# Kernel optimization log

Hardware: AMD Instinct MI355X
Metric: run time of the kernel (lower is better)

## Reference

```python
import jax, jax.numpy as jnp
import numpy as np

N = 100000      # number of nodes
E = 1600000     # number of (directed) edges, avg degree 16
DIN = 128       # in_features
DOUT = 32       # out_features
SLOPE = 0.2     # leaky relu negative slope


def setup_inputs() -> dict:
    key = jax.random.key(0)
    k1, k2, k3, k4, k5, k6 = jax.random.split(key, 6)
    x = jax.random.normal(k1, (N, DIN), dtype=jnp.float32)
    edge_index = jax.random.randint(k2, (2, E), 0, N, dtype=jnp.int32)
    # W1 (shared with W2 and used as the feature-update matrix W, 'source' mode)
    W1_w = jax.random.normal(k3, (DOUT, DIN), dtype=jnp.float32) / np.float32(np.sqrt(DIN))
    W1_b = jax.random.normal(k4, (DOUT,), dtype=jnp.float32) * 0.01
    a1_w = jax.random.normal(k5, (DOUT,), dtype=jnp.float32) / np.float32(np.sqrt(DOUT))
    a2_w = jax.random.normal(k6, (DOUT,), dtype=jnp.float32) / np.float32(np.sqrt(DOUT))
    return {"x": x, "edge_index": edge_index, "W1_w": W1_w, "W1_b": W1_b,
            "a1_w": a1_w, "a2_w": a2_w}


def reference(x, edge_index, W1_w, W1_b, a1_w, a2_w):
    n = x.shape[0]
    # append self-loops, as in _sparse_attention
    loops = jnp.arange(n, dtype=edge_index.dtype)
    src = jnp.concatenate([edge_index[0], loops])   # rows  (softmax segments)
    dst = jnp.concatenate([edge_index[1], loops])   # cols
    # h = W1(x) (linear, with bias); W2 = W1 (weight sharing), W = W2 ('source')
    h = x @ W1_w.T + W1_b                           # [N, DOUT]
    z = jax.nn.leaky_relu(h, SLOPE)                 # x1 == x2 under weight sharing
    s1 = z @ a1_w                                   # [N] per-node src score
    s2 = z @ a2_w                                   # [N] per-node dst score
    logits = s1[src] + s2[dst]                      # [E+N] per-edge attention logit
    # row-wise (dim=1) sparse softmax == segment softmax over src
    m = jax.ops.segment_max(logits, src, num_segments=n)
    ex = jnp.exp(logits - m[src])
    denom = jax.ops.segment_sum(ex, src, num_segments=n)
    alpha = ex / denom[src]                         # normalized attention per edge
    # sparse-dense matmul: out[i] = sum_{(i,j)} alpha_ij * h[j]
    return jax.ops.segment_sum(alpha[:, None] * h[dst], src, num_segments=n)
```

## Files before the change

kernel.cpp:

```cpp
#include <hip/hip_runtime.h>
#include <hip/hip_fp16.h>

#define DIN 128
#define DOUT 32
#define SLOPE 0.2f

#define BSHIFT 7
#define BNODES 128
#define NBS    1024
#define BPITCH 784
#define CAP    3072
#define TILE   4096
#define EPB    (TILE / 256)
#define TPW    4

typedef short s16x8 __attribute__((ext_vector_type(8)));
typedef float f32x4 __attribute__((ext_vector_type(4)));

__device__ __forceinline__ short f2bf(float f) {
    unsigned u = __float_as_uint(f);
    return (short)((u + 0x7fffu + ((u >> 16) & 1u)) >> 16);
}
__device__ __forceinline__ float bf2f(short s) {
    return __uint_as_float(((unsigned)(unsigned short)s) << 16);
}

__device__ __forceinline__ void linear_role(
    int wid, int ntiles, int lane, int N,
    const float* __restrict__ x, const float* __restrict__ W,
    const float* __restrict__ b, const float* __restrict__ a2,
    __half* __restrict__ g16, float* __restrict__ es2)
{
    if (wid * TPW >= ntiles) return;
    int m = lane & 15, oct = lane >> 4;

    s16x8 bh[2][4], bl[2][4];
    #pragma unroll
    for (int t = 0; t < 2; ++t) {
        const float* wrow = W + (long)(t * 16 + m) * DIN + oct * 8;
        #pragma unroll
        for (int kc = 0; kc < 4; ++kc) {
            float4 w0 = *(const float4*)(wrow + kc * 32);
            float4 w1 = *(const float4*)(wrow + kc * 32 + 4);
            float wf[8] = {w0.x, w0.y, w0.z, w0.w, w1.x, w1.y, w1.z, w1.w};
            #pragma unroll
            for (int j = 0; j < 8; ++j) {
                short hh = f2bf(wf[j]);
                bh[t][kc][j] = hh;
                bl[t][kc][j] = f2bf(wf[j] - bf2f(hh));
            }
        }
    }

    int c0 = m, c1 = 16 + m;
    float b0 = b[c0], b1 = b[c1], A0 = a2[c0], A1 = a2[c1];

    #pragma unroll 1
    for (int g = 0; g < TPW; ++g) {
        int tile = wid * TPW + g;
        if (tile >= ntiles) break;
        long rowbase = (long)tile * 16;

        long lrow = rowbase + m; if (lrow > N - 1) lrow = N - 1;
        const float* xrow = x + lrow * DIN + oct * 8;
        f32x4 acc0 = {0.f, 0.f, 0.f, 0.f}, acc1 = {0.f, 0.f, 0.f, 0.f};
        #pragma unroll
        for (int kc = 0; kc < 4; ++kc) {
            float4 x0 = *(const float4*)(xrow + kc * 32);
            float4 x1 = *(const float4*)(xrow + kc * 32 + 4);
            float xf[8] = {x0.x, x0.y, x0.z, x0.w, x1.x, x1.y, x1.z, x1.w};
            s16x8 ah, al;
            #pragma unroll
            for (int j = 0; j < 8; ++j) {
                short hh = f2bf(xf[j]);
                ah[j] = hh;
                al[j] = f2bf(xf[j] - bf2f(hh));
            }
            acc0 = __builtin_amdgcn_mfma_f32_16x16x32_bf16(al, bh[0][kc], acc0, 0, 0, 0);
            acc0 = __builtin_amdgcn_mfma_f32_16x16x32_bf16(ah, bl[0][kc], acc0, 0, 0, 0);
            acc0 = __builtin_amdgcn_mfma_f32_16x16x32_bf16(ah, bh[0][kc], acc0, 0, 0, 0);
            acc1 = __builtin_amdgcn_mfma_f32_16x16x32_bf16(al, bh[1][kc], acc1, 0, 0, 0);
            acc1 = __builtin_amdgcn_mfma_f32_16x16x32_bf16(ah, bl[1][kc], acc1, 0, 0, 0);
            acc1 = __builtin_amdgcn_mfma_f32_16x16x32_bf16(ah, bh[1][kc], acc1, 0, 0, 0);
        }

        float hv0[4], hv1[4], sp[4];
        #pragma unroll
        for (int i = 0; i < 4; ++i) {
            hv0[i] = acc0[i] + b0;
            hv1[i] = acc1[i] + b1;
            float z0 = hv0[i] > 0.f ? hv0[i] : SLOPE * hv0[i];
            float z1 = hv1[i] > 0.f ? hv1[i] : SLOPE * hv1[i];
            sp[i] = z0 * A0 + z1 * A1;
        }
        #pragma unroll
        for (int off = 1; off <= 8; off <<= 1) {
            #pragma unroll
            for (int i = 0; i < 4; ++i) sp[i] += __shfl_xor(sp[i], off, 64);
        }
        #pragma unroll
        for (int i = 0; i < 4; ++i) {
            long r = rowbase + oct * 4 + i;
            if (r >= N) continue;
            float ev = __expf(sp[i]);
            g16[r * DOUT + c0] = __float2half(ev * hv0[i]);
            g16[r * DOUT + c1] = __float2half(ev * hv1[i]);
            if (m == 0) es2[r] = ev;
        }
    }
}

__global__ __launch_bounds__(256) void gat_fused(
    const float* __restrict__ x, const float* __restrict__ W,
    const float* __restrict__ b, const float* __restrict__ a2,
    const int* __restrict__ src, const int* __restrict__ dst,
    __half* __restrict__ g16, float* __restrict__ es2,
    unsigned* __restrict__ ebuf, int* __restrict__ boff,
    int N, int E, int ntiles, int nbin)
{
    if ((int)blockIdx.x >= nbin) {
        int wave = threadIdx.x >> 6;
        int wid = (blockIdx.x - nbin) * 4 + wave;
        linear_role(wid, ntiles, threadIdx.x & 63, N, x, W, b, a2, g16, es2);
        return;
    }
    __shared__ int cnt[NBS];
    __shared__ int offs[NBS];
    __shared__ int wsum[4], wbase[4];
    int tid = threadIdx.x;
    long tstart = (long)blockIdx.x * TILE;

    for (int i = tid; i < NBS; i += 256) cnt[i] = 0;
    __syncthreads();

    unsigned rec[EPB];
    int      bq[EPB];
    #pragma unroll
    for (int it = 0; it < EPB; ++it) {
        long e = tstart + it * 256 + tid;
        int s = (e < E) ? src[e] : -1;
        int d = (e < E) ? dst[e] : 0;
        if (s >= 0) {
            int bk = s >> BSHIFT;
            int rv = atomicAdd(&cnt[bk], 1);
            rec[it] = ((unsigned)(s & (BNODES - 1)) << 17) | (unsigned)d;
            bq[it] = (rv < 511) ? ((bk << 9) | rv) : -1;
        } else bq[it] = -1;
    }
    __syncthreads();

    int t4 = tid << 2;
    int c0 = cnt[t4], c1 = cnt[t4 + 1], c2 = cnt[t4 + 2], c3 = cnt[t4 + 3];
    int s4 = c0 + c1 + c2 + c3;
    int v = s4;
    #pragma unroll
    for (int off = 1; off < 64; off <<= 1) {
        int t = __shfl_up(v, off, 64);
        if ((tid & 63) >= off) v += t;
    }
    if ((tid & 63) == 63) wsum[tid >> 6] = v;
    __syncthreads();
    if (tid == 0) {
        int a = 0;
        #pragma unroll
        for (int w = 0; w < 4; ++w) { wbase[w] = a; a += wsum[w]; }
    }
    __syncthreads();
    int base = wbase[tid >> 6] + (v - s4);
    offs[t4]     = base;
    offs[t4 + 1] = base + c0;
    offs[t4 + 2] = base + c0 + c1;
    offs[t4 + 3] = base + c0 + c1 + c2;
    __syncthreads();

    for (int i = tid; i < BPITCH - 1; i += 256)
        boff[(size_t)blockIdx.x * BPITCH + i] = offs[i];
    if (tid == 0)
        boff[(size_t)blockIdx.x * BPITCH + BPITCH - 1] = offs[BPITCH - 1];

    #pragma unroll
    for (int it = 0; it < EPB; ++it) {
        int q = bq[it];
        if (q >= 0) {
            int pos = offs[q >> 9] + (q & 511);
            ebuf[tstart + pos] = rec[it];
        }
    }
}

__global__ __launch_bounds__(512) void gat_aggregate(
    const __half* __restrict__ g16, const float* __restrict__ es2,
    const unsigned* __restrict__ ebuf, const int* __restrict__ boff,
    float* __restrict__ out, int N, int nbin)
{
    __shared__ unsigned rs[CAP];
    __shared__ unsigned srt[CAP];
    __shared__ int cnt[BNODES];
    __shared__ int sc[BNODES];
    __shared__ int basep[BNODES];
    __shared__ int pos2[BNODES];
    __shared__ int wsum[8], wbase[8], totsh;
    int tid = threadIdx.x;

    int nwg = gridDim.x;
    int xcd = blockIdx.x & 7;
    int q = nwg >> 3, rr = nwg & 7;
    int bk = (xcd < rr ? xcd * (q + 1) : rr * (q + 1) + (xcd - rr) * q)
           + ((int)blockIdx.x >> 3);

    if (tid < BNODES) { cnt[tid] = 0; pos2[tid] = 0; }
    __syncthreads();

    int rstart = 0, rlen = 0;
    if (tid < nbin) {
        const int* row = boff + (size_t)tid * BPITCH + bk;
        rstart = row[0];
        rlen   = row[1] - rstart;
    }
    int v = rlen;
    #pragma unroll
    for (int off = 1; off < 64; off <<= 1) {
        int t = __shfl_up(v, off, 64);
        if ((tid & 63) >= off) v += t;
    }
    if ((tid & 63) == 63) wsum[tid >> 6] = v;
    __syncthreads();
    if (tid == 0) {
        int a = 0;
        #pragma unroll
        for (int w = 0; w < 8; ++w) { wbase[w] = a; a += wsum[w]; }
        totsh = a;
    }
    __syncthreads();
    int dest = wbase[tid >> 6] + (v - rlen);
    int lim = CAP - dest; if (lim < 0) lim = 0;
    if (rlen > lim) rlen = lim;
    {
        const unsigned* seg = ebuf + (size_t)tid * TILE + rstart;
        for (int j = 0; j < rlen; ++j) {
            unsigned u = seg[j];
            rs[dest + j] = u;
            atomicAdd(&cnt[u >> 17], 1);
        }
    }
    __syncthreads();
    int cntb = totsh; if (cntb > CAP) cntb = CAP;

    if (tid < BNODES) sc[tid] = cnt[tid];
    __syncthreads();
    #pragma unroll
    for (int off = 1; off < BNODES; off <<= 1) {
        int t = (tid >= off && tid < BNODES) ? sc[tid - off] : 0;
        __syncthreads();
        if (tid < BNODES) sc[tid] += t;
        __syncthreads();
    }
    if (tid < BNODES) basep[tid] = sc[tid] - cnt[tid];
    __syncthreads();
    for (int r = tid; r < cntb; r += 512) {
        unsigned u = rs[r];
        int sl = (int)(u >> 17);
        int p = basep[sl] + atomicAdd(&pos2[sl], 1);
        srt[p] = u & 0x1FFFFu;
    }
    __syncthreads();

    int unit = tid >> 5, col = tid & 31;
    for (int sl = unit; sl < BNODES; sl += 16) {
        long node = (long)bk * BNODES + sl;
        if (node >= N) break;
        float acc = __half2float(g16[node * DOUT + col]);
        float d = es2[node];
        int e = basep[sl], e_end = basep[sl] + cnt[sl];

        while (e + 8 <= e_end) {
            int dn[8];
            #pragma unroll
            for (int j = 0; j < 8; ++j) dn[j] = (int)srt[e + j];
            unsigned short gv[8];
            #pragma unroll
            for (int j = 0; j < 8; ++j)
                gv[j] = *(const unsigned short*)&g16[(long)dn[j] * DOUT + col];
            float ev[8];
            #pragma unroll
            for (int j = 0; j < 8; ++j) ev[j] = es2[dn[j]];
            #pragma unroll
            for (int j = 0; j < 8; ++j) {
                acc += __half2float(*(const __half*)&gv[j]);
                d += ev[j];
            }
            e += 8;
        }
        while (e + 4 <= e_end) {
            int dn[4];
            #pragma unroll
            for (int j = 0; j < 4; ++j) dn[j] = (int)srt[e + j];
            unsigned short gv[4];
            #pragma unroll
            for (int j = 0; j < 4; ++j)
                gv[j] = *(const unsigned short*)&g16[(long)dn[j] * DOUT + col];
            float ev[4];
            #pragma unroll
            for (int j = 0; j < 4; ++j) ev[j] = es2[dn[j]];
            #pragma unroll
            for (int j = 0; j < 4; ++j) {
                acc += __half2float(*(const __half*)&gv[j]);
                d += ev[j];
            }
            e += 4;
        }
        for (; e < e_end; ++e) {
            int dn = (int)srt[e];
            acc += __half2float(g16[(long)dn * DOUT + col]);
            d += es2[dn];
        }
        out[node * DOUT + col] = acc / d;
    }
}

extern "C" void kernel_launch(void* const* d_in, const int* in_sizes, int n_in,
                              void* d_out, int out_size, void* d_ws, size_t ws_size,
                              hipStream_t stream)
{
    const float* x  = (const float*)d_in[0];
    const int*   ei = (const int*)d_in[1];
    const float* W  = (const float*)d_in[2];
    const float* b  = (const float*)d_in[3];
    const float* a2 = (const float*)d_in[5];
    float* out = (float*)d_out;

    int N = in_sizes[0] / DIN;
    int E = in_sizes[1] / 2;
    const int* src = ei;
    const int* dst = ei + E;

    int NB = (N + BNODES - 1) >> BSHIFT;
    int nbin = (E + TILE - 1) / TILE;

    char* ws = (char*)d_ws;
    __half*   g16  = (__half*)ws;   ws += (size_t)N * DOUT * sizeof(__half);
    float*    es2  = (float*)ws;    ws += (size_t)N * sizeof(float);
    int*      boff = (int*)ws;      ws += (size_t)nbin * BPITCH * sizeof(int);
    unsigned* ebuf = (unsigned*)ws; ws += (size_t)nbin * TILE * sizeof(unsigned);

    int ntiles = (N + 15) / 16;
    int nwaves = (ntiles + TPW - 1) / TPW;
    int nlin   = (nwaves + 3) / 4;

    gat_fused    <<<nbin + nlin, 256, 0, stream>>>(x, W, b, a2, src, dst,
                                                   g16, es2, ebuf, boff,
                                                   N, E, ntiles, nbin);
    gat_aggregate<<<NB, 512, 0, stream>>>(g16, es2, ebuf, boff, out, N, nbin);
}
```

Measured before the change: 157.2 us.

## Transpose bin offset table and gather edge records in parallel per block

The per-tile bin offset table is now stored transposed (bin-major, padded pitch), so each aggregate block reads its start and end offsets from contiguous memory instead of strided rows. The serial per-thread copy of edge records into shared memory is replaced by building an address list and then doing a strided parallel gather into registers, which spreads the global loads across all threads. The 128-entry block scan with many barriers is replaced by a single-wave shuffle scan. In exchange the producer does scattered writes when storing the transposed offsets, and the gather adds an extra shared-memory address pass.

```diff
diff --git a/kernel.cpp b/kernel.cpp
--- a/kernel.cpp
+++ b/kernel.cpp
@@ -8,7 +8,6 @@
 #define BSHIFT 7
 #define BNODES 128
 #define NBS    1024
-#define BPITCH 784
 #define CAP    3072
 #define TILE   4096
 #define EPB    (TILE / 256)
@@ -115,8 +114,8 @@
     const float* __restrict__ b, const float* __restrict__ a2,
     const int* __restrict__ src, const int* __restrict__ dst,
     __half* __restrict__ g16, float* __restrict__ es2,
-    unsigned* __restrict__ ebuf, int* __restrict__ boff,
-    int N, int E, int ntiles, int nbin)
+    unsigned* __restrict__ ebuf, int* __restrict__ boffT,
+    int N, int E, int ntiles, int nbin, int nbinp)
 {
     if ((int)blockIdx.x >= nbin) {
         int wave = threadIdx.x >> 6;
@@ -173,10 +172,9 @@
     offs[t4 + 3] = base + c0 + c1 + c2;
     __syncthreads();
 
-    for (int i = tid; i < BPITCH - 1; i += 256)
-        boff[(size_t)blockIdx.x * BPITCH + i] = offs[i];
-    if (tid == 0)
-        boff[(size_t)blockIdx.x * BPITCH + BPITCH - 1] = offs[BPITCH - 1];
+    int NBv = (N + BNODES - 1) >> BSHIFT;
+    for (int i = tid; i <= NBv; i += 256)
+        boffT[(size_t)i * nbinp + blockIdx.x] = offs[i];
 
     #pragma unroll
     for (int it = 0; it < EPB; ++it) {
@@ -190,13 +188,12 @@
 
 __global__ __launch_bounds__(512) void gat_aggregate(
     const __half* __restrict__ g16, const float* __restrict__ es2,
-    const unsigned* __restrict__ ebuf, const int* __restrict__ boff,
-    float* __restrict__ out, int N, int nbin)
+    const unsigned* __restrict__ ebuf, const int* __restrict__ boffT,
+    float* __restrict__ out, int N, int nbin, int nbinp)
 {
-    __shared__ unsigned rs[CAP];
     __shared__ unsigned srt[CAP];
+    __shared__ unsigned srca[CAP];
     __shared__ int cnt[BNODES];
-    __shared__ int sc[BNODES];
     __shared__ int basep[BNODES];
     __shared__ int pos2[BNODES];
     __shared__ int wsum[8], wbase[8], totsh;
@@ -209,13 +206,11 @@
            + ((int)blockIdx.x >> 3);
 
     if (tid < BNODES) { cnt[tid] = 0; pos2[tid] = 0; }
-    __syncthreads();
 
     int rstart = 0, rlen = 0;
     if (tid < nbin) {
-        const int* row = boff + (size_t)tid * BPITCH + bk;
-        rstart = row[0];
-        rlen   = row[1] - rstart;
+        rstart = boffT[(size_t)bk * nbinp + tid];
+        rlen   = boffT[(size_t)(bk + 1) * nbinp + tid] - rstart;
     }
     int v = rlen;
     #pragma unroll
@@ -236,32 +231,50 @@
     int lim = CAP - dest; if (lim < 0) lim = 0;
     if (rlen > lim) rlen = lim;
     {
-        const unsigned* seg = ebuf + (size_t)tid * TILE + rstart;
-        for (int j = 0; j < rlen; ++j) {
-            unsigned u = seg[j];
-            rs[dest + j] = u;
-            atomicAdd(&cnt[u >> 17], 1);
-        }
+        unsigned abase = (unsigned)tid * TILE + (unsigned)rstart;
+        for (int j = 0; j < rlen; ++j)
+            srca[dest + j] = abase + (unsigned)j;
     }
     __syncthreads();
     int cntb = totsh; if (cntb > CAP) cntb = CAP;
 
-    if (tid < BNODES) sc[tid] = cnt[tid];
-    __syncthreads();
-    #pragma unroll
-    for (int off = 1; off < BNODES; off <<= 1) {
-        int t = (tid >= off && tid < BNODES) ? sc[tid - off] : 0;
-        __syncthreads();
-        if (tid < BNODES) sc[tid] += t;
-        __syncthreads();
-    }
-    if (tid < BNODES) basep[tid] = sc[tid] - cnt[tid];
-    __syncthreads();
-    for (int r = tid; r < cntb; r += 512) {
-        unsigned u = rs[r];
-        int sl = (int)(u >> 17);
-        int p = basep[sl] + atomicAdd(&pos2[sl], 1);
-        srt[p] = u & 0x1FFFFu;
+    unsigned held[6];
+    #pragma unroll
+    for (int k = 0; k < 6; ++k) {
+        int r = tid + (k << 9);
+        held[k] = 0xFFFFFFFFu;
+        if (r < cntb) held[k] = ebuf[(size_t)srca[r]];
+    }
+    #pragma unroll
+    for (int k = 0; k < 6; ++k) {
+        unsigned u = held[k];
+        if (u != 0xFFFFFFFFu) atomicAdd(&cnt[u >> 17], 1);
+    }
+    __syncthreads();
+
+    if (tid < 64) {
+        int a = cnt[2 * tid], b2 = cnt[2 * tid + 1];
+        int s = a + b2;
+        int vv = s;
+        #pragma unroll
+        for (int off = 1; off < 64; off <<= 1) {
+            int t = __shfl_up(vv, off, 64);
+            if (tid >= off) vv += t;
+        }
+        int excl = vv - s;
+        basep[2 * tid]     = excl;
+        basep[2 * tid + 1] = excl + a;
+    }
+    __syncthreads();
+
+    #pragma unroll
+    for (int k = 0; k < 6; ++k) {
+        unsigned u = held[k];
+        if (u != 0xFFFFFFFFu) {
+            int sl = (int)(u >> 17);
+            int p = basep[sl] + atomicAdd(&pos2[sl], 1);
+            srt[p] = u & 0x1FFFFu;
+        }
     }
     __syncthreads();
 
@@ -336,19 +349,21 @@
 
     int NB = (N + BNODES - 1) >> BSHIFT;
     int nbin = (E + TILE - 1) / TILE;
+    int nbinp = (nbin + 7) & ~7;
 
     char* ws = (char*)d_ws;
-    __half*   g16  = (__half*)ws;   ws += (size_t)N * DOUT * sizeof(__half);
-    float*    es2  = (float*)ws;    ws += (size_t)N * sizeof(float);
-    int*      boff = (int*)ws;      ws += (size_t)nbin * BPITCH * sizeof(int);
-    unsigned* ebuf = (unsigned*)ws; ws += (size_t)nbin * TILE * sizeof(unsigned);
+    __half*   g16   = (__half*)ws;  ws += (size_t)N * DOUT * sizeof(__half);
+    float*    es2   = (float*)ws;   ws += (size_t)N * sizeof(float);
+    int*      boffT = (int*)ws;     ws += (size_t)(NB + 1) * nbinp * sizeof(int);
+    unsigned* ebuf  = (unsigned*)ws; ws += (size_t)nbin * TILE * sizeof(unsigned);
 
     int ntiles = (N + 15) / 16;
     int nwaves = (ntiles + TPW - 1) / TPW;
     int nlin   = (nwaves + 3) / 4;
 
     gat_fused    <<<nbin + nlin, 256, 0, stream>>>(x, W, b, a2, src, dst,
-                                                   g16, es2, ebuf, boff,
-                                                   N, E, ntiles, nbin);
-    gat_aggregate<<<NB, 512, 0, stream>>>(g16, es2, ebuf, boff, out, N, nbin);
-}
+                                                   g16, es2, ebuf, boffT,
+                                                   N, E, ntiles, nbin, nbinp);
+    gat_aggregate<<<NB, 512, 0, stream>>>(g16, es2, ebuf, boffT, out, N,
+                                          nbin, nbinp);
+}
```

After: 154.1 us. 1.02x faster.
